# Kernel optimization log

Hardware: AMD Instinct MI355X
Metric: run time of the kernel (lower is better)

Reference implementation:

```python
import jax, jax.numpy as jnp
import numpy as np

N = 131072  # nodes processed in one frontier/level batch
H = 256     # h_size
X = 256     # x_size


def setup_inputs() -> dict:
    key = jax.random.key(0)
    ks = jax.random.split(key, 8)
    def w(k, shape, fan_in):
        return jax.random.normal(k, shape, jnp.float32) / np.float32(np.sqrt(fan_in))
    return {
        "x": jax.random.normal(ks[0], (N, X), jnp.float32),
        "child_h": jax.random.normal(ks[1], (N, H), jnp.float32),
        "child_c": jax.random.normal(ks[2], (N, H), jnp.float32),
        "child_idx": jax.random.randint(ks[3], (N,), 0, N, jnp.int32),
        "W_iou_w": w(ks[4], (3 * H, X), X),
        "U_iou_w": w(ks[5], (3 * H, H), H),
        "b_iou": jnp.zeros((1, 3 * H), jnp.float32),
        "W_f_w": w(ks[6], (H, X), X),
        "W_f_b": jnp.zeros((H,), jnp.float32),
        "U_f_w": w(ks[7], (H, H), H),
        "U_f_b": jnp.zeros((H,), jnp.float32),
        "b_f": jnp.zeros((1, H), jnp.float32),
    }


def reference(x, child_h, child_c, child_idx, W_iou_w, U_iou_w, b_iou,
              W_f_w, W_f_b, U_f_w, U_f_b, b_f):
    # Node-local projections (precomputed 'Wx' / 'Wfx' node data in the DGL module)
    Wx = x @ W_iou_w.T                      # [N, 3H]
    Wfx = x @ W_f_w.T + W_f_b               # [N, H] (nn.Linear bias included)
    # message_func + mailbox gather (one child per node; see shape analysis)
    hc = child_h[child_idx]                 # [N, H] irregular gather
    cc = child_c[child_idx]                 # [N, H]
    # reduce_func: forget gate + masked sum over children (K=1)
    f = jax.nn.sigmoid(Wfx + hc @ U_f_w.T + U_f_b + b_f)  # [N, H]
    c_red = f * cc                          # sum over 1 child
    iou = Wx + b_iou + hc @ U_iou_w.T       # [N, 3H]
    # apply_node_func: gated combine
    i, o, u = jnp.split(iou, 3, axis=1)
    c = jax.nn.sigmoid(i) * jnp.tanh(u) + c_red
    h = jax.nn.sigmoid(o) * jnp.tanh(c)
    return h, c
```

## Files before the change

### kernel.cpp

```cpp
#include <hip/hip_runtime.h>


typedef unsigned short u16;
typedef unsigned int u32;
typedef __bf16 bf16x8 __attribute__((ext_vector_type(8)));
typedef float f32x16 __attribute__((ext_vector_type(16)));
typedef u16 u16x4 __attribute__((ext_vector_type(4)));
typedef u16 u16x8 __attribute__((ext_vector_type(8)));

#define NTOT 131072
#define NHOFF (131072 * 256)

__device__ __forceinline__ u16 f2bf(float f) {
  u32 u = __float_as_uint(f);
  return (u16)((u + 0x7FFFu + ((u >> 16) & 1u)) >> 16);
}

__global__ void prep_w(const float* __restrict__ Wiou, const float* __restrict__ Uiou,
                       const float* __restrict__ Wf, const float* __restrict__ Uf,
                       u16* __restrict__ Bpack) {
  int cid = blockIdx.x * 256 + threadIdx.x;
  int j = cid >> 6;
  int kc = cid & 63;
  int k = kc * 8;
  int kt = kc >> 3, k8 = kc & 7;
  int s = j >> 8, g = (j >> 6) & 3, e = j & 63;
  int c = s * 64 + e;
  const float* src;
  if (j < 768) src = (k < 256) ? (Wiou + j * 256 + k) : (Uiou + j * 256 + (k - 256));
  else { int jj = j - 768; src = (k < 256) ? (Wf + jj * 256 + k) : (Uf + jj * 256 + (k - 256)); }
  float4 f0 = *(const float4*)(src);
  float4 f1 = *(const float4*)(src + 4);
  u16x8 v;
  v[0] = f2bf(f0.x); v[1] = f2bf(f0.y); v[2] = f2bf(f0.z); v[3] = f2bf(f0.w);
  v[4] = f2bf(f1.x); v[5] = f2bf(f1.y); v[6] = f2bf(f1.z); v[7] = f2bf(f1.w);
  int slot = (g * 8 + kt) * 2048 + ((c * 8 + k8) ^ (c & 7));
  *(u16x8*)(Bpack + slot * 8) = v;
}

__global__ void prep_bias(const float* __restrict__ biou, const float* __restrict__ wfb,
                          const float* __restrict__ ufb, const float* __restrict__ bfv,
                          float* __restrict__ Bias) {
  int j = blockIdx.x * 256 + threadIdx.x;
  Bias[j] = (j < 768) ? biou[j] : (wfb[j - 768] + ufb[j - 768] + bfv[j - 768]);
}

__global__ void prep_apack(const float* __restrict__ x, const float* __restrict__ ch,
                           const int* __restrict__ cidx, u16* __restrict__ Apack) {
  int e = blockIdx.x * 256 + threadIdx.x;
  int n = e >> 6, c = e & 63;
  const float* src = (c < 32) ? (x + (size_t)n * 256 + c * 8)
                              : (ch + (size_t)cidx[n] * 256 + (c - 32) * 8);
  float4 f0 = *(const float4*)src;
  float4 f1 = *(const float4*)(src + 4);
  u16x8 v;
  v[0] = f2bf(f0.x); v[1] = f2bf(f0.y); v[2] = f2bf(f0.z); v[3] = f2bf(f0.w);
  v[4] = f2bf(f1.x); v[5] = f2bf(f1.y); v[6] = f2bf(f1.z); v[7] = f2bf(f1.w);
  *(u16x8*)(Apack + (size_t)n * 512 + c * 8) = v;
}

__global__ __launch_bounds__(256, 2)
void treelstm_main_bf16(const u16* __restrict__ Apack, const u16* __restrict__ Bpack,
                        const float* __restrict__ Bias, const float* __restrict__ child_c,
                        const int* __restrict__ cidx, float* __restrict__ out) {
  __shared__ __align__(16) u16 ldsA[128 * 64];
  __shared__ __align__(16) u16 ldsB[256 * 64];
  __shared__ int lds_cidx[128];

  const int tid = threadIdx.x;
  const int n0 = blockIdx.x * 128;
  const int g = blockIdx.y;

  if (tid < 128) lds_cidx[tid] = cidx[n0 + tid];

  const int lane = tid & 63, w = tid >> 6;
  const int wm = w >> 1, wn = w & 1;
  const int lr = lane & 31, hi = lane >> 5;

  f32x16 acc[2][4] = {};

  const char* aP = (const char*)Apack
      + (size_t)(n0 + w * 32 + (lane >> 3)) * 1024
      + (((lane & 7) ^ ((lane >> 3) & 7)) << 4);
  const char* bP = (const char*)Bpack + (size_t)g * 262144 + ((w * 512 + lane) << 4);

  char* ldsAw = (char*)ldsA + w * 4096;
  char* ldsBw = (char*)ldsB + w * 8192;

  const char* ldsAb = (const char*)ldsA;
  const char* ldsBb = (const char*)ldsB;
  int arow[2];
  #pragma unroll
  for (int mi = 0; mi < 2; mi++) arow[mi] = (wm * 64 + mi * 32 + lr) * 128;
  const int aswz = (lr & 7) << 4;
  int brow[4];
  #pragma unroll
  for (int s = 0; s < 4; s++) brow[s] = (s * 64 + wn * 32 + lr) * 128;
  const int bswz = (lr & 7) << 4;

  #pragma unroll 1
  for (int kt = 0; kt < 8; ++kt) {
    #pragma unroll
    for (int q = 0; q < 4; ++q)
      __builtin_amdgcn_global_load_lds(
          (const __attribute__((address_space(1))) void*)(aP + q * 8192),
          (__attribute__((address_space(3))) void*)(ldsAw + q * 1024), 16, 0, 0);
    #pragma unroll
    for (int q = 0; q < 8; ++q)
      __builtin_amdgcn_global_load_lds(
          (const __attribute__((address_space(1))) void*)(bP + q * 1024),
          (__attribute__((address_space(3))) void*)(ldsBw + q * 1024), 16, 0, 0);
    __syncthreads();
    #pragma unroll
    for (int ks = 0; ks < 4; ++ks) {
      int kb = ks * 32 + hi * 16;
      bf16x8 af[2], bfr[4];
      #pragma unroll
      for (int mi = 0; mi < 2; mi++)
        af[mi] = *(const bf16x8*)(ldsAb + ((arow[mi] + kb) ^ aswz));
      #pragma unroll
      for (int s = 0; s < 4; s++)
        bfr[s] = *(const bf16x8*)(ldsBb + ((brow[s] + kb) ^ bswz));
      #pragma unroll
      for (int mi = 0; mi < 2; mi++)
        #pragma unroll
        for (int s = 0; s < 4; s++)
          acc[mi][s] = __builtin_amdgcn_mfma_f32_32x32x16_bf16(af[mi], bfr[s], acc[mi][s], 0, 0, 0);
    }
    __syncthreads();
    aP += 128;
    bP += 32768;
  }

  const int tcol = g * 64 + wn * 32 + lr;
  const float bi = Bias[tcol], bo = Bias[256 + tcol], bu = Bias[512 + tcol], bfg = Bias[768 + tcol];
  #pragma unroll
  for (int mi = 0; mi < 2; mi++) {
    #pragma unroll
    for (int reg = 0; reg < 16; ++reg) {
      int row = wm * 64 + mi * 32 + (reg & 3) + 8 * (reg >> 2) + 4 * hi;
      int n = n0 + row;
      float i_ = acc[mi][0][reg] + bi;
      float o_ = acc[mi][1][reg] + bo;
      float u_ = acc[mi][2][reg] + bu;
      float fp = acc[mi][3][reg] + bfg;
      float ccv = child_c[(size_t)lds_cidx[row] * 256 + tcol];
      float sigi = 1.f / (1.f + __expf(-i_));
      float sigo = 1.f / (1.f + __expf(-o_));
      float sigf = 1.f / (1.f + __expf(-fp));
      float tu = 2.f / (1.f + __expf(-2.f * u_)) - 1.f;
      float c = sigi * tu + sigf * ccv;
      float tc = 2.f / (1.f + __expf(-2.f * c)) - 1.f;
      out[(size_t)n * 256 + tcol] = sigo * tc;
      out[NHOFF + (size_t)n * 256 + tcol] = c;
    }
  }
}

__global__ __launch_bounds__(256, 2)
void treelstm_main_f32(const float* __restrict__ x, const float* __restrict__ child_h,
                       const float* __restrict__ child_c, const int* __restrict__ cidx,
                       const u16* __restrict__ Bpack, const float* __restrict__ Bias,
                       float* __restrict__ out) {
  __shared__ __align__(16) u16 ldsA[128 * 64];
  __shared__ __align__(16) u16 ldsB[256 * 64];
  __shared__ int lds_cidx[128];

  const int tid = threadIdx.x;
  const int n0 = blockIdx.x * 128;
  const int g = blockIdx.y;

  if (tid < 128) lds_cidx[tid] = cidx[n0 + tid];

  const int lane = tid & 63, w = tid >> 6;
  const int wm = w >> 1, wn = w & 1;
  const int lr = lane & 31, hi = lane >> 5;

  f32x16 acc[2][4] = {};

  const char* ldsAb = (const char*)ldsA;
  const char* ldsBb = (const char*)ldsB;
  int arow[2];
  #pragma unroll
  for (int mi = 0; mi < 2; mi++) arow[mi] = (wm * 64 + mi * 32 + lr) * 128;
  const int aswz = (lr & 7) << 4;
  int brow[4];
  #pragma unroll
  for (int s = 0; s < 4; s++) brow[s] = (s * 64 + wn * 32 + lr) * 128;
  const int bswz = (lr & 7) << 4;

  for (int kt = 0; kt < 8; ++kt) {
    #pragma unroll
    for (int q = 0; q < 8; ++q) {
      int v = q * 256 + tid;
      int r = v >> 4;
      int kq = (v & 15) * 4;
      const float* src = (kt < 4) ? (x + (size_t)(n0 + r) * 256 + kt * 64 + kq)
                                  : (child_h + (size_t)lds_cidx[r] * 256 + (kt - 4) * 64 + kq);
      float4 d = *(const float4*)src;
      u16x4 b;
      b[0] = f2bf(d.x); b[1] = f2bf(d.y); b[2] = f2bf(d.z); b[3] = f2bf(d.w);
      int addr = (r * 128 + kq * 2) ^ ((r & 7) << 4);
      *(u16x4*)((char*)ldsA + addr) = b;
    }
    const u16* bsrc = Bpack + (g * 8 + kt) * 16384;
    #pragma unroll
    for (int q = 0; q < 8; ++q) {
      int m = q * 256 + tid;
      *(u16x8*)((char*)ldsB + m * 16) = *(const u16x8*)(bsrc + m * 8);
    }
    __syncthreads();
    #pragma unroll
    for (int ks = 0; ks < 4; ++ks) {
      int kb = ks * 32 + hi * 16;
      bf16x8 af[2], bfr[4];
      #pragma unroll
      for (int mi = 0; mi < 2; mi++)
        af[mi] = *(const bf16x8*)(ldsAb + ((arow[mi] + kb) ^ aswz));
      #pragma unroll
      for (int s = 0; s < 4; s++)
        bfr[s] = *(const bf16x8*)(ldsBb + ((brow[s] + kb) ^ bswz));
      #pragma unroll
      for (int mi = 0; mi < 2; mi++)
        #pragma unroll
        for (int s = 0; s < 4; s++)
          acc[mi][s] = __builtin_amdgcn_mfma_f32_32x32x16_bf16(af[mi], bfr[s], acc[mi][s], 0, 0, 0);
    }
    __syncthreads();
  }

  const int tcol = g * 64 + wn * 32 + lr;
  const float bi = Bias[tcol], bo = Bias[256 + tcol], bu = Bias[512 + tcol], bfg = Bias[768 + tcol];
  #pragma unroll
  for (int mi = 0; mi < 2; mi++) {
    #pragma unroll
    for (int reg = 0; reg < 16; ++reg) {
      int row = wm * 64 + mi * 32 + (reg & 3) + 8 * (reg >> 2) + 4 * hi;
      int n = n0 + row;
      float i_ = acc[mi][0][reg] + bi;
      float o_ = acc[mi][1][reg] + bo;
      float u_ = acc[mi][2][reg] + bu;
      float fp = acc[mi][3][reg] + bfg;
      float ccv = child_c[(size_t)lds_cidx[row] * 256 + tcol];
      float sigi = 1.f / (1.f + __expf(-i_));
      float sigo = 1.f / (1.f + __expf(-o_));
      float sigf = 1.f / (1.f + __expf(-fp));
      float tu = 2.f / (1.f + __expf(-2.f * u_)) - 1.f;
      float c = sigi * tu + sigf * ccv;
      float tc = 2.f / (1.f + __expf(-2.f * c)) - 1.f;
      out[(size_t)n * 256 + tcol] = sigo * tc;
      out[NHOFF + (size_t)n * 256 + tcol] = c;
    }
  }
}

extern "C" void kernel_launch(void* const* d_in, const int* in_sizes, int n_in,
                              void* d_out, int out_size, void* d_ws, size_t ws_size,
                              hipStream_t stream) {
  const float* x    = (const float*)d_in[0];
  const float* ch   = (const float*)d_in[1];
  const float* cc   = (const float*)d_in[2];
  const int*   ci   = (const int*)d_in[3];
  const float* Wiou = (const float*)d_in[4];
  const float* Uiou = (const float*)d_in[5];
  const float* biou = (const float*)d_in[6];
  const float* Wf   = (const float*)d_in[7];
  const float* Wfb  = (const float*)d_in[8];
  const float* Uf   = (const float*)d_in[9];
  const float* Ufb  = (const float*)d_in[10];
  const float* bfv  = (const float*)d_in[11];

  u16* Bpack = (u16*)d_ws;
  float* Bias = (float*)((char*)d_ws + (1 << 20));
  u16* Apack = (u16*)((char*)d_ws + (2 << 20));

  const size_t need = (size_t)(2 << 20) + (size_t)NTOT * 512 * sizeof(u16);

  prep_w<<<256, 256, 0, stream>>>(Wiou, Uiou, Wf, Uf, Bpack);
  prep_bias<<<4, 256, 0, stream>>>(biou, Wfb, Ufb, bfv, Bias);

  dim3 grid(1024, 4);
  if (ws_size >= need) {
    prep_apack<<<32768, 256, 0, stream>>>(x, ch, ci, Apack);
    treelstm_main_bf16<<<grid, 256, 0, stream>>>(Apack, Bpack, Bias, cc, ci, (float*)d_out);
  } else {
    treelstm_main_f32<<<grid, 256, 0, stream>>>(x, ch, cc, ci, Bpack, Bias, (float*)d_out);
  }
}
```

Baseline: 318.6 us.

## Use triple-buffered 256-row tiles with B fragments loaded directly from global

```diff
diff --git a/kernel.cpp b/kernel.cpp
--- a/kernel.cpp
+++ b/kernel.cpp
@@ -9,16 +9,39 @@
 typedef u16 u16x8 __attribute__((ext_vector_type(8)));
 
 #define NTOT 131072
-#define NHOFF (131072 * 256)
+#define NHOFF ((size_t)131072 * 256)
 
 __device__ __forceinline__ u16 f2bf(float f) {
   u32 u = __float_as_uint(f);
   return (u16)((u + 0x7FFFu + ((u >> 16) & 1u)) >> 16);
 }
 
-__global__ void prep_w(const float* __restrict__ Wiou, const float* __restrict__ Uiou,
-                       const float* __restrict__ Wf, const float* __restrict__ Uf,
-                       u16* __restrict__ Bpack) {
+__global__ void prep_w_frag(const float* __restrict__ Wiou, const float* __restrict__ Uiou,
+                            const float* __restrict__ Wf, const float* __restrict__ Uf,
+                            u16* __restrict__ BpackF) {
+  int c = blockIdx.x * 256 + threadIdx.x;
+  int np = c & 255;
+  int r = c >> 8;
+  int hi = r & 1; r >>= 1;
+  int ks = r & 3; r >>= 2;
+  int kt = r & 7; r >>= 3;
+  int g  = r & 3;
+  int j = (np >> 6) * 256 + g * 64 + (np & 63);
+  int k0 = kt * 64 + ks * 16 + hi * 8;
+  const float* src;
+  if (j < 768) src = (k0 < 256) ? (Wiou + (size_t)j * 256 + k0) : (Uiou + (size_t)j * 256 + (k0 - 256));
+  else { int jj = j - 768; src = (k0 < 256) ? (Wf + (size_t)jj * 256 + k0) : (Uf + (size_t)jj * 256 + (k0 - 256)); }
+  float4 f0 = *(const float4*)(src);
+  float4 f1 = *(const float4*)(src + 4);
+  u16x8 v;
+  v[0] = f2bf(f0.x); v[1] = f2bf(f0.y); v[2] = f2bf(f0.z); v[3] = f2bf(f0.w);
+  v[4] = f2bf(f1.x); v[5] = f2bf(f1.y); v[6] = f2bf(f1.z); v[7] = f2bf(f1.w);
+  *(u16x8*)(BpackF + (size_t)c * 8) = v;
+}
+
+__global__ void prep_w_legacy(const float* __restrict__ Wiou, const float* __restrict__ Uiou,
+                              const float* __restrict__ Wf, const float* __restrict__ Uf,
+                              u16* __restrict__ Bpack) {
   int cid = blockIdx.x * 256 + threadIdx.x;
   int j = cid >> 6;
   int kc = cid & 63;
@@ -59,10 +82,110 @@
   *(u16x8*)(Apack + (size_t)n * 512 + c * 8) = v;
 }
 
+__global__ __launch_bounds__(512, 2)
+void treelstm_main8(const u16* __restrict__ Apack, const u16* __restrict__ BpackF,
+                    const float* __restrict__ Bias, const float* __restrict__ child_c,
+                    const int* __restrict__ cidx, float* __restrict__ out) {
+  __shared__ __align__(16) u16 ring[3 * 16384];
+  __shared__ int lds_cidx[256];
+
+  const int tid = threadIdx.x;
+  const int n0 = blockIdx.x * 256;
+  const int g = blockIdx.y;
+  if (tid < 256) lds_cidx[tid] = cidx[n0 + tid];
+
+  const int lane = tid & 63, w = tid >> 6;
+  const int wm = w >> 1, wn = w & 1;
+  const int lr = lane & 31, hi = lane >> 5;
+
+  const u16* aSrc = Apack + (size_t)(n0 + (tid >> 3)) * 512
+                    + (((tid & 7) ^ ((tid >> 3) & 7)) << 3);
+  const u16* bP = BpackF + (size_t)g * 131072 + (size_t)hi * 2048 + (size_t)(wn * 32 + lr) * 8;
+
+  u16* bufs[3] = {ring, ring + 16384, ring + 32768};
+
+  int arowb[2];
+  #pragma unroll
+  for (int mi = 0; mi < 2; mi++) arowb[mi] = (wm * 64 + mi * 32 + lr) * 128;
+  const int aswz = (lr & 7) << 4;
+  const int hib = hi * 16;
+
+  f32x16 acc[2][4] = {};
+
+  #define STAGE(T, BUF)                                                              \
+    { _Pragma("unroll") for (int q = 0; q < 4; ++q)                                  \
+        __builtin_amdgcn_global_load_lds(                                            \
+            (const __attribute__((address_space(1))) void*)(aSrc + (T) * 64 + q * 32768), \
+            (__attribute__((address_space(3))) void*)((BUF) + q * 4096 + w * 512),   \
+            16, 0, 0); }
+
+  STAGE(0, bufs[0]);
+  STAGE(1, bufs[1]);
+
+  #pragma unroll
+  for (int t = 0; t < 8; ++t) {
+    __builtin_amdgcn_sched_barrier(0);
+    asm volatile("s_waitcnt vmcnt(0) lgkmcnt(0)\n\ts_barrier" ::: "memory");
+    __builtin_amdgcn_sched_barrier(0);
+    if (t < 6) STAGE(t + 2, bufs[(t + 2) % 3]);
+    bf16x8 bfr[4][4];
+    #pragma unroll
+    for (int nf = 0; nf < 4; ++nf)
+      #pragma unroll
+      for (int ks = 0; ks < 4; ++ks)
+        bfr[nf][ks] = *(const bf16x8*)(bP + (size_t)t * 16384 + ks * 4096 + nf * 512);
+    const char* cur = (const char*)bufs[t % 3];
+    bf16x8 afr[2][4];
+    #pragma unroll
+    for (int mi = 0; mi < 2; ++mi)
+      #pragma unroll
+      for (int ks = 0; ks < 4; ++ks)
+        afr[mi][ks] = *(const bf16x8*)(cur + arowb[mi] + ((ks * 32 + hib) ^ aswz));
+    __builtin_amdgcn_s_setprio(1);
+    #pragma unroll
+    for (int ks = 0; ks < 4; ++ks)
+      #pragma unroll
+      for (int mi = 0; mi < 2; ++mi)
+        #pragma unroll
+        for (int nf = 0; nf < 4; ++nf)
+          acc[mi][nf] = __builtin_amdgcn_mfma_f32_32x32x16_bf16(afr[mi][ks], bfr[nf][ks],
+                                                                acc[mi][nf], 0, 0, 0);
+    __builtin_amdgcn_s_setprio(0);
+  }
+  #undef STAGE
+
+  const int hcol = g * 64 + wn * 32 + lr;
+  float b4[4];
+  #pragma unroll
+  for (int nf = 0; nf < 4; ++nf) b4[nf] = Bias[nf * 256 + hcol];
+  #pragma unroll
+  for (int mi = 0; mi < 2; ++mi) {
+    #pragma unroll
+    for (int reg = 0; reg < 16; ++reg) {
+      int rowb = wm * 64 + mi * 32 + (reg & 3) + 8 * (reg >> 2) + 4 * hi;
+      size_t n = (size_t)(n0 + rowb);
+      float i_ = acc[mi][0][reg] + b4[0];
+      float o_ = acc[mi][1][reg] + b4[1];
+      float u_ = acc[mi][2][reg] + b4[2];
+      float fp = acc[mi][3][reg] + b4[3];
+      float ccv = child_c[(size_t)lds_cidx[rowb] * 256 + hcol];
+      float sigi = 1.f / (1.f + __expf(-i_));
+      float sigo = 1.f / (1.f + __expf(-o_));
+      float sigf = 1.f / (1.f + __expf(-fp));
+      float tu = 2.f / (1.f + __expf(-2.f * u_)) - 1.f;
+      float c = sigi * tu + sigf * ccv;
+      float tc = 2.f / (1.f + __expf(-2.f * c)) - 1.f;
+      out[n * 256 + hcol] = sigo * tc;
+      out[NHOFF + n * 256 + hcol] = c;
+    }
+  }
+}
+
 __global__ __launch_bounds__(256, 2)
-void treelstm_main_bf16(const u16* __restrict__ Apack, const u16* __restrict__ Bpack,
-                        const float* __restrict__ Bias, const float* __restrict__ child_c,
-                        const int* __restrict__ cidx, float* __restrict__ out) {
+void treelstm_main_f32(const float* __restrict__ x, const float* __restrict__ child_h,
+                       const float* __restrict__ child_c, const int* __restrict__ cidx,
+                       const u16* __restrict__ Bpack, const float* __restrict__ Bias,
+                       float* __restrict__ out) {
   __shared__ __align__(16) u16 ldsA[128 * 64];
   __shared__ __align__(16) u16 ldsB[256 * 64];
   __shared__ int lds_cidx[128];
@@ -79,14 +202,6 @@
 
   f32x16 acc[2][4] = {};
 
-  const char* aP = (const char*)Apack
-      + (size_t)(n0 + w * 32 + (lane >> 3)) * 1024
-      + (((lane & 7) ^ ((lane >> 3) & 7)) << 4);
-  const char* bP = (const char*)Bpack + (size_t)g * 262144 + ((w * 512 + lane) << 4);
-
-  char* ldsAw = (char*)ldsA + w * 4096;
-  char* ldsBw = (char*)ldsB + w * 8192;
-
   const char* ldsAb = (const char*)ldsA;
   const char* ldsBb = (const char*)ldsB;
   int arow[2];
@@ -98,18 +213,26 @@
   for (int s = 0; s < 4; s++) brow[s] = (s * 64 + wn * 32 + lr) * 128;
   const int bswz = (lr & 7) << 4;
 
-  #pragma unroll 1
   for (int kt = 0; kt < 8; ++kt) {
     #pragma unroll
-    for (int q = 0; q < 4; ++q)
-      __builtin_amdgcn_global_load_lds(
-          (const __attribute__((address_space(1))) void*)(aP + q * 8192),
-          (__attribute__((address_space(3))) void*)(ldsAw + q * 1024), 16, 0, 0);
-    #pragma unroll
-    for (int q = 0; q < 8; ++q)
-      __builtin_amdgcn_global_load_lds(
-          (const __attribute__((address_space(1))) void*)(bP + q * 1024),
-          (__attribute__((address_space(3))) void*)(ldsBw + q * 1024), 16, 0, 0);
+    for (int q = 0; q < 8; ++q) {
+      int v = q * 256 + tid;
+      int r = v >> 4;
+      int kq = (v & 15) * 4;
+      const float* src = (kt < 4) ? (x + (size_t)(n0 + r) * 256 + kt * 64 + kq)
+                                  : (child_h + (size_t)lds_cidx[r] * 256 + (kt - 4) * 64 + kq);
+      float4 d = *(const float4*)src;
+      u16x4 b;
+      b[0] = f2bf(d.x); b[1] = f2bf(d.y); b[2] = f2bf(d.z); b[3] = f2bf(d.w);
+      int addr = (r * 128 + kq * 2) ^ ((r & 7) << 4);
+      *(u16x4*)((char*)ldsA + addr) = b;
+    }
+    const u16* bsrc = Bpack + (g * 8 + kt) * 16384;
+    #pragma unroll
+    for (int q = 0; q < 8; ++q) {
+      int m = q * 256 + tid;
+      *(u16x8*)((char*)ldsB + m * 16) = *(const u16x8*)(bsrc + m * 8);
+    }
     __syncthreads();
     #pragma unroll
     for (int ks = 0; ks < 4; ++ks) {
@@ -128,8 +251,6 @@
           acc[mi][s] = __builtin_amdgcn_mfma_f32_32x32x16_bf16(af[mi], bfr[s], acc[mi][s], 0, 0, 0);
     }
     __syncthreads();
-    aP += 128;
-    bP += 32768;
   }
 
   const int tcol = g * 64 + wn * 32 + lr;
@@ -157,103 +278,6 @@
   }
 }
 
-__global__ __launch_bounds__(256, 2)
-void treelstm_main_f32(const float* __restrict__ x, const float* __restrict__ child_h,
-                       const float* __restrict__ child_c, const int* __restrict__ cidx,
-                       const u16* __restrict__ Bpack, const float* __restrict__ Bias,
-                       float* __restrict__ out) {
-  __shared__ __align__(16) u16 ldsA[128 * 64];
-  __shared__ __align__(16) u16 ldsB[256 * 64];
-  __shared__ int lds_cidx[128];
-
-  const int tid = threadIdx.x;
-  const int n0 = blockIdx.x * 128;
-  const int g = blockIdx.y;
-
-  if (tid < 128) lds_cidx[tid] = cidx[n0 + tid];
-
-  const int lane = tid & 63, w = tid >> 6;
-  const int wm = w >> 1, wn = w & 1;
-  const int lr = lane & 31, hi = lane >> 5;
-
-  f32x16 acc[2][4] = {};
-
-  const char* ldsAb = (const char*)ldsA;
-  const char* ldsBb = (const char*)ldsB;
-  int arow[2];
-  #pragma unroll
-  for (int mi = 0; mi < 2; mi++) arow[mi] = (wm * 64 + mi * 32 + lr) * 128;
-  const int aswz = (lr & 7) << 4;
-  int brow[4];
-  #pragma unroll
-  for (int s = 0; s < 4; s++) brow[s] = (s * 64 + wn * 32 + lr) * 128;
-  const int bswz = (lr & 7) << 4;
-
-  for (int kt = 0; kt < 8; ++kt) {
-    #pragma unroll
-    for (int q = 0; q < 8; ++q) {
-      int v = q * 256 + tid;
-      int r = v >> 4;
-      int kq = (v & 15) * 4;
-      const float* src = (kt < 4) ? (x + (size_t)(n0 + r) * 256 + kt * 64 + kq)
-                                  : (child_h + (size_t)lds_cidx[r] * 256 + (kt - 4) * 64 + kq);
-      float4 d = *(const float4*)src;
-      u16x4 b;
-      b[0] = f2bf(d.x); b[1] = f2bf(d.y); b[2] = f2bf(d.z); b[3] = f2bf(d.w);
-      int addr = (r * 128 + kq * 2) ^ ((r & 7) << 4);
-      *(u16x4*)((char*)ldsA + addr) = b;
-    }
-    const u16* bsrc = Bpack + (g * 8 + kt) * 16384;
-    #pragma unroll
-    for (int q = 0; q < 8; ++q) {
-      int m = q * 256 + tid;
-      *(u16x8*)((char*)ldsB + m * 16) = *(const u16x8*)(bsrc + m * 8);
-    }
-    __syncthreads();
-    #pragma unroll
-    for (int ks = 0; ks < 4; ++ks) {
-      int kb = ks * 32 + hi * 16;
-      bf16x8 af[2], bfr[4];
-      #pragma unroll
-      for (int mi = 0; mi < 2; mi++)
-        af[mi] = *(const bf16x8*)(ldsAb + ((arow[mi] + kb) ^ aswz));
-      #pragma unroll
-      for (int s = 0; s < 4; s++)
-        bfr[s] = *(const bf16x8*)(ldsBb + ((brow[s] + kb) ^ bswz));
-      #pragma unroll
-      for (int mi = 0; mi < 2; mi++)
-        #pragma unroll
-        for (int s = 0; s < 4; s++)
-          acc[mi][s] = __builtin_amdgcn_mfma_f32_32x32x16_bf16(af[mi], bfr[s], acc[mi][s], 0, 0, 0);
-    }
-    __syncthreads();
-  }
-
-  const int tcol = g * 64 + wn * 32 + lr;
-  const float bi = Bias[tcol], bo = Bias[256 + tcol], bu = Bias[512 + tcol], bfg = Bias[768 + tcol];
-  #pragma unroll
-  for (int mi = 0; mi < 2; mi++) {
-    #pragma unroll
-    for (int reg = 0; reg < 16; ++reg) {
-      int row = wm * 64 + mi * 32 + (reg & 3) + 8 * (reg >> 2) + 4 * hi;
-      int n = n0 + row;
-      float i_ = acc[mi][0][reg] + bi;
-      float o_ = acc[mi][1][reg] + bo;
-      float u_ = acc[mi][2][reg] + bu;
-      float fp = acc[mi][3][reg] + bfg;
-      float ccv = child_c[(size_t)lds_cidx[row] * 256 + tcol];
-      float sigi = 1.f / (1.f + __expf(-i_));
-      float sigo = 1.f / (1.f + __expf(-o_));
-      float sigf = 1.f / (1.f + __expf(-fp));
-      float tu = 2.f / (1.f + __expf(-2.f * u_)) - 1.f;
-      float c = sigi * tu + sigf * ccv;
-      float tc = 2.f / (1.f + __expf(-2.f * c)) - 1.f;
-      out[(size_t)n * 256 + tcol] = sigo * tc;
-      out[NHOFF + (size_t)n * 256 + tcol] = c;
-    }
-  }
-}
-
 extern "C" void kernel_launch(void* const* d_in, const int* in_sizes, int n_in,
                               void* d_out, int out_size, void* d_ws, size_t ws_size,
                               hipStream_t stream) {
@@ -276,14 +300,16 @@
 
   const size_t need = (size_t)(2 << 20) + (size_t)NTOT * 512 * sizeof(u16);
 
-  prep_w<<<256, 256, 0, stream>>>(Wiou, Uiou, Wf, Uf, Bpack);
   prep_bias<<<4, 256, 0, stream>>>(biou, Wfb, Ufb, bfv, Bias);
 
-  dim3 grid(1024, 4);
   if (ws_size >= need) {
+    prep_w_frag<<<256, 256, 0, stream>>>(Wiou, Uiou, Wf, Uf, Bpack);
     prep_apack<<<32768, 256, 0, stream>>>(x, ch, ci, Apack);
-    treelstm_main_bf16<<<grid, 256, 0, stream>>>(Apack, Bpack, Bias, cc, ci, (float*)d_out);
+    dim3 grid(512, 4);
+    treelstm_main8<<<grid, 512, 0, stream>>>(Apack, Bpack, Bias, cc, ci, (float*)d_out);
   } else {
+    prep_w_legacy<<<256, 256, 0, stream>>>(Wiou, Uiou, Wf, Uf, Bpack);
+    dim3 grid(1024, 4);
     treelstm_main_f32<<<grid, 256, 0, stream>>>(x, ch, cc, ci, Bpack, Bias, (float*)d_out);
   }
 }
```

Result: slower. 367.2 us (+15.2%).
